# Kernel optimization log

Hardware: AMD Instinct MI355X
Metric: run time of the kernel (lower is better)

Reference implementation:

```python
import jax, jax.numpy as jnp
import numpy as np

B, L, D = 1, 4096, 1024
H = 16
HD = D // H
SCALE = HD ** -0.5


def setup_inputs() -> dict:
    key = jax.random.key(0)
    k1, k2, k3 = jax.random.split(key, 3)
    X = jax.random.normal(k1, (B, L, D), dtype=jnp.float32)
    # torch Linear default init ~ U(-1/sqrt(fan_in), 1/sqrt(fan_in)); scaled normals are fine for a reference
    Wqkv = jax.random.normal(k2, (D, 3 * D), dtype=jnp.float32) * (D ** -0.5)
    bqkv = jnp.zeros((3 * D,), dtype=jnp.float32)
    Wproj = jax.random.normal(k3, (D, D), dtype=jnp.float32) * (D ** -0.5)
    bproj = jnp.zeros((D,), dtype=jnp.float32)
    return {"X": X, "Wqkv": Wqkv, "bqkv": bqkv, "Wproj": Wproj, "bproj": bproj}


def reference(X, Wqkv, bqkv, Wproj, bproj):
    Bn, Ln, Dn = X.shape
    qkv = X @ Wqkv + bqkv                       # [B, L, 3D]
    qkv = qkv.reshape(Bn, Ln, 3, H, HD)
    q, k, v = qkv[:, :, 0], qkv[:, :, 1], qkv[:, :, 2]   # [B, L, H, HD]
    # attention scores [B, H, L, L] (naive, matches original)
    attn = jnp.einsum('bqhd,bkhd->bhqk', q, k) * SCALE
    causal = jnp.tril(jnp.ones((Ln, Ln), dtype=bool))     # True = keep
    attn = jnp.where(causal, attn, -jnp.inf)
    score = jax.nn.softmax(attn, axis=-1)
    out = jnp.einsum('bhqk,bkhd->bqhd', score, v)         # [B, L, H, HD]
    out = out.reshape(Bn, Ln, Dn)
    return out @ Wproj + bproj
```

## Files before the change

### kernel.cpp

```cpp
#include <hip/hip_runtime.h>
#include <hip/hip_bf16.h>
#include <string.h>


typedef unsigned short ushort_t;
typedef __attribute__((ext_vector_type(8))) short short8;
typedef __attribute__((ext_vector_type(4))) short short4_t;
typedef __attribute__((ext_vector_type(4))) float f32x4;

#define MFMA16(a, b, c) __builtin_amdgcn_mfma_f32_16x16x32_bf16(a, b, c, 0, 0, 0)

#if __has_builtin(__builtin_amdgcn_mfma_f32_16x16x16bf16_1k)
#define HAVE_MFMA16K 1
__device__ __forceinline__ f32x4 mfma16x16(short4_t a, short4_t b, f32x4 c) {
    return __builtin_amdgcn_mfma_f32_16x16x16bf16_1k(a, b, c, 0, 0, 0);
}
#else
#define HAVE_MFMA16K 0
__device__ __forceinline__ f32x4 mfma16x16(short4_t a, short4_t b, f32x4 c) {
    asm("s_nop 1\n\tv_mfma_f32_16x16x16_bf16 %0, %1, %2, %0"
        : "+v"(c) : "v"(a), "v"(b));
    return c;
}
#endif

static constexpr int Lq = 4096;
static constexpr int Dm = 1024;
static constexpr int NH = 16;
static constexpr int HD = 64;
static constexpr int D3 = 3072;
static constexpr float SCALE_LOG2E = 0.125f * 1.44269504088896340736f;

__device__ __forceinline__ ushort_t f2bf(float f) {
    union { float f; unsigned int u; } x{f};
    unsigned int u = x.u;
    u += 0x7fffu + ((u >> 16) & 1u);
    return (ushort_t)(u >> 16);
}

__device__ __forceinline__ unsigned int cvtpk(float a, float b) {
    __hip_bfloat162 h = __float22bfloat162_rn(make_float2(a, b));
    unsigned int u;
    memcpy(&u, &h, 4);
    return u;
}

__device__ __forceinline__ void gl2lds16(const ushort_t* g, ushort_t* l) {
    __builtin_amdgcn_global_load_lds(
        (const __attribute__((address_space(1))) unsigned int*)g,
        (__attribute__((address_space(3))) unsigned int*)l, 16, 0, 0);
}

__global__ void __launch_bounds__(256)
prep(const float* __restrict__ X, const float* __restrict__ Wqkv,
     const float* __restrict__ Wproj, ushort_t* __restrict__ Xb,
     ushort_t* __restrict__ WqkvT, ushort_t* __restrict__ WprojT) {
    __shared__ float tile[32][33];
    const int bid = blockIdx.x, tid = threadIdx.x;
    if (bid < 4096) {
        int i = (bid * 256 + tid) * 4;
        float4 v = *(const float4*)&X[i];
        ushort_t r[4] = { f2bf(v.x), f2bf(v.y), f2bf(v.z), f2bf(v.w) };
        *(uint2*)&Xb[i] = *(uint2*)r;
        return;
    }
    const float* W; ushort_t* Wt; int Nd, nb, kb;
    if (bid < 7168) {
        int b = bid - 4096; W = Wqkv;  Wt = WqkvT;  Nd = 3072;
        nb = (b % 96) * 32; kb = (b / 96) * 32;
    } else {
        int b = bid - 7168; W = Wproj; Wt = WprojT; Nd = 1024;
        nb = (b % 32) * 32; kb = (b / 32) * 32;
    }
    const int tx = tid & 31, ty = tid >> 5;
    for (int j = 0; j < 32; j += 8)
        tile[ty + j][tx] = W[(size_t)(kb + ty + j) * Nd + nb + tx];
    __syncthreads();
    for (int j = 0; j < 32; j += 8)
        Wt[(size_t)(nb + ty + j) * Dm + kb + tx] = f2bf(tile[tx][ty + j]);
}

__global__ void __launch_bounds__(256)
gemm_qkv(const ushort_t* __restrict__ A, const ushort_t* __restrict__ Bt,
         const float* __restrict__ bias, ushort_t* __restrict__ Cq,
         ushort_t* __restrict__ Vt) {
    __shared__ alignas(16) ushort_t Alds[128 * 32];
    __shared__ alignas(16) ushort_t Blds[128 * 32];
    const int tid  = threadIdx.x;
    const int lane = tid & 63;
    const int w    = tid >> 6;
    const int quad = lane >> 4;
    const int l16  = lane & 15;
    const int mbase = blockIdx.x * 128;
    const int nbase = blockIdx.y * 128;
    const int moff  = (w >> 1) * 64;
    const int noff  = (w & 1) * 64;
    const int K = Dm;

    f32x4 acc[4][4] = {};

    for (int kb = 0; kb < K; kb += 32) {
        __syncthreads();
        #pragma unroll
        for (int c = 0; c < 2; c++) {
            int id  = w * 128 + c * 64 + lane;
            int row = id >> 2, col = (id & 3) * 8;
            gl2lds16(&A[(size_t)(mbase + row) * K + kb + col], &Alds[(size_t)(w * 128 + c * 64) * 8]);
            gl2lds16(&Bt[(size_t)(nbase + row) * K + kb + col], &Blds[(size_t)(w * 128 + c * 64) * 8]);
        }
        __syncthreads();
        short8 a[4], b[4];
        #pragma unroll
        for (int m = 0; m < 4; m++)
            a[m] = *(const short8*)&Alds[(moff + m * 16 + l16) * 32 + quad * 8];
        #pragma unroll
        for (int n = 0; n < 4; n++)
            b[n] = *(const short8*)&Blds[(noff + n * 16 + l16) * 32 + quad * 8];
        #pragma unroll
        for (int m = 0; m < 4; m++)
            #pragma unroll
            for (int n = 0; n < 4; n++)
                acc[m][n] = MFMA16(a[m], b[n], acc[m][n]);
    }

    if (nbase < 2048) {
        const bool qscale = (nbase < 1024);
        #pragma unroll
        for (int m = 0; m < 4; m++)
            #pragma unroll
            for (int n = 0; n < 4; n++)
                #pragma unroll
                for (int r = 0; r < 4; r++) {
                    int row = mbase + moff + m * 16 + quad * 4 + r;
                    int col = nbase + noff + n * 16 + l16;
                    float v = acc[m][n][r] + bias[col];
                    if (qscale) v *= SCALE_LOG2E;
                    Cq[(size_t)row * D3 + col] = f2bf(v);
                }
    } else {
        const int dbase = nbase - 2048 + noff;
        const size_t kb0 = (size_t)mbase + moff;
        #pragma unroll
        for (int n = 0; n < 4; n++) {
            const float bv = bias[nbase + noff + n * 16 + l16];
            ushort_t* vrow = Vt + (size_t)(dbase + n * 16 + l16) * Lq + kb0 + quad * 16;
            #pragma unroll
            for (int rp = 0; rp < 2; rp++) {
                ushort_t pk[8];
                #pragma unroll
                for (int dr = 0; dr < 2; dr++)
                    #pragma unroll
                    for (int m = 0; m < 4; m++)
                        pk[dr * 4 + m] = f2bf(acc[m][n][2 * rp + dr] + bv);
                *(short8*)(vrow + rp * 8) = *(const short8*)pk;
            }
        }
    }
}

__global__ void __launch_bounds__(1024)
attn_fwd(const ushort_t* __restrict__ qkv, const ushort_t* __restrict__ Vt,
         ushort_t* __restrict__ O) {
    union SMem {
        struct { ushort_t K[2][2][64 * 64]; ushort_t V[2][2][64 * 64]; } kv;
        float Ml[3 * 256 * 35];
    };
    __shared__ SMem sm;

    const int tid  = threadIdx.x;
    const int lane = tid & 63;
    const int w    = tid >> 6;
    const int qtr  = w >> 2;
    const int sub  = w & 3;
    const int quad = lane >> 4;
    const int l16  = lane & 15;
    const int bid  = blockIdx.x;
    const int h    = bid & 15;
    const int p    = bid >> 4;
    const float NEG_INF = -__builtin_inff();

    const ushort_t* kbase = qkv + Dm + h * HD;
    const ushort_t* vbase = Vt + (size_t)h * HD * Lq;

    int koff[2][2];
    #pragma unroll
    for (int s = 0; s < 2; s++) {
        const int tok = (l16 & 3) * 16 + (qtr & 1) * 8 + s * 4 + (l16 >> 2);
        const int fk  = ((l16 & 3) << 1) | ((l16 >> 2) & 1);
        #pragma unroll
        for (int kh = 0; kh < 2; kh++)
            koff[s][kh] = tok * 64 + (((kh * 4 + quad) ^ fk) * 8);
    }
    int voff[4][2];
    #pragma unroll
    for (int t4 = 0; t4 < 4; t4++)
        #pragma unroll
        for (int s = 0; s < 2; s++) {
            const int row = t4 * 16 + l16;
            const int g = (qtr & 1) * 4 + s * 2 + (quad >> 1);
            voff[t4][s] = row * 64 + ((g ^ (l16 & 7)) * 8) + (quad & 1) * 4;
        }
    const int kmc = (qtr >> 1) * 64 + (qtr & 1) * 8 + quad;

    const int  tv  = tid & 511;
    const int  rr  = tv >> 3;
    const int  ccK = (tv & 7) ^ ((((rr >> 4) & 3) << 1) | (rr & 1));
    const int  ccV = (tv & 7) ^ (rr & 7);
    const bool isK = (tid < 512);
    const int  dsto = (w & 7) * 512;
    const ushort_t* kse = kbase + (size_t)rr * D3 + ccK * 8;
    const ushort_t* vse = vbase + (size_t)rr * Lq + ccV * 8;

    for (int sel = 0; sel < 2; sel++) {
        const int c      = sel ? (31 - p) : p;
        const int qc     = c * 128;
        const int rounds = c + 1;
        const int qrow0  = qc + sub * 32;

        short8 qf[2][2];
        #pragma unroll
        for (int m = 0; m < 2; m++) {
            const ushort_t* qr = qkv + (size_t)(qrow0 + m * 16 + l16) * D3 + h * HD;
            qf[m][0] = *(const short8*)(qr + quad * 8);
            qf[m][1] = *(const short8*)(qr + 32 + quad * 8);
        }

        f32x4 o[2][4] = {};
        float sacc[2] = { 0.f, 0.f };

        const ushort_t* kp = kse;
        const ushort_t* vp = vse;

        auto stage = [&](int b) {
            if (isK) {
                gl2lds16(kp,           &sm.kv.K[0][b][dsto]);
                gl2lds16(kp + 64 * D3, &sm.kv.K[1][b][dsto]);
            } else {
                gl2lds16(vp,           &sm.kv.V[0][b][dsto]);
                gl2lds16(vp + 64,      &sm.kv.V[1][b][dsto]);
            }
            kp += (size_t)128 * D3;
            vp += 128;
        };

        stage(0);

        for (int r = 0; r < rounds; r++) {
            const int buf = r & 1;
            __syncthreads();
            if (r + 1 < rounds) stage(buf ^ 1);

            const ushort_t* Kb = &sm.kv.K[qtr >> 1][buf][0];
            const ushort_t* Vb = &sm.kv.V[qtr >> 1][buf][0];
            const bool domask = (r == rounds - 1);

            short8 kf[2][2];
            #pragma unroll
            for (int s = 0; s < 2; s++)
                #pragma unroll
                for (int kh = 0; kh < 2; kh++)
                    kf[s][kh] = *(const short8*)&Kb[koff[s][kh]];

            short4_t pT[2][2];
            #pragma unroll
            for (int m = 0; m < 2; m++) {
                const int qg = qrow0 + m * 16 + l16;
                #pragma unroll
                for (int s = 0; s < 2; s++) {
                    f32x4 t = {};
                    t = MFMA16(kf[s][0], qf[m][0], t);
                    t = MFMA16(kf[s][1], qf[m][1], t);
                    float e[4];
                    #pragma unroll
                    for (int r4 = 0; r4 < 4; r4++) {
                        float v = t[r4];
                        if (domask && (r * 128 + kmc + s * 4 + r4 * 16 > qg))
                            v = NEG_INF;
                        e[r4] = __builtin_amdgcn_exp2f(v);
                    }
                    sacc[m] += (e[0] + e[1]) + (e[2] + e[3]);
                    union { unsigned int u[2]; short4_t s4; } pb;
                    pb.u[0] = cvtpk(e[0], e[1]);
                    pb.u[1] = cvtpk(e[2], e[3]);
                    pT[m][s] = pb.s4;
                }
            }

            #pragma unroll
            for (int t4 = 0; t4 < 4; t4++)
                #pragma unroll
                for (int s = 0; s < 2; s++) {
                    short4_t vf = *(const short4_t*)&Vb[voff[t4][s]];
                    o[0][t4] = mfma16x16(vf, pT[0][s], o[0][t4]);
                    o[1][t4] = mfma16x16(vf, pT[1][s], o[1][t4]);
                }
        }

#if !HAVE_MFMA16K
        asm volatile("s_nop 7\n\ts_nop 7" ::: "memory");
#endif
        #pragma unroll
        for (int m = 0; m < 2; m++) {
            sacc[m] += __shfl_xor(sacc[m], 16);
            sacc[m] += __shfl_xor(sacc[m], 32);
        }

        __syncthreads();
        if (qtr != 0) {
            float* dst = sm.Ml + (size_t)((qtr - 1) * 256 + sub * 64 + lane) * 35;
            #pragma unroll
            for (int m = 0; m < 2; m++)
                #pragma unroll
                for (int t4 = 0; t4 < 4; t4++)
                    *(f32x4*)(dst + (m * 4 + t4) * 4) = o[m][t4];
            dst[32] = sacc[0];
            dst[33] = sacc[1];
        }
        __syncthreads();
        if (qtr == 0) {
            #pragma unroll
            for (int j = 0; j < 3; j++) {
                const float* src = sm.Ml + (size_t)(j * 256 + sub * 64 + lane) * 35;
                #pragma unroll
                for (int m = 0; m < 2; m++)
                    #pragma unroll
                    for (int t4 = 0; t4 < 4; t4++)
                        o[m][t4] += *(const f32x4*)(src + (m * 4 + t4) * 4);
                sacc[0] += src[32];
                sacc[1] += src[33];
            }
            #pragma unroll
            for (int m = 0; m < 2; m++) {
                const float inv = 1.0f / sacc[m];
                ushort_t* orow = O + (size_t)(qrow0 + m * 16 + l16) * Dm + h * HD;
                #pragma unroll
                for (int t4 = 0; t4 < 4; t4++) {
                    ushort_t pk[4];
                    #pragma unroll
                    for (int r4 = 0; r4 < 4; r4++)
                        pk[r4] = f2bf(o[m][t4][r4] * inv);
                    *(uint2*)(orow + t4 * 16 + quad * 4) = *(const uint2*)pk;
                }
            }
        }
        __syncthreads();
    }
}

__global__ void __launch_bounds__(256)
gemm_proj(const ushort_t* __restrict__ A, const ushort_t* __restrict__ Bt,
          const float* __restrict__ bias, float* __restrict__ C) {
    __shared__ alignas(16) ushort_t Alds[128 * 32];
    __shared__ alignas(16) ushort_t Blds[64 * 32];
    const int tid  = threadIdx.x;
    const int lane = tid & 63;
    const int w    = tid >> 6;
    const int quad = lane >> 4;
    const int l16  = lane & 15;
    const int mbase = blockIdx.x * 128;
    const int nbase = blockIdx.y * 64;
    const int moff  = (w >> 1) * 64;
    const int noff  = (w & 1) * 32;
    const int K = Dm, N = Dm;

    f32x4 acc[4][2] = {};

    for (int kb = 0; kb < K; kb += 32) {
        __syncthreads();
        #pragma unroll
        for (int c = 0; c < 2; c++) {
            int id  = w * 128 + c * 64 + lane;
            int row = id >> 2, col = (id & 3) * 8;
            gl2lds16(&A[(size_t)(mbase + row) * K + kb + col], &Alds[(size_t)(w * 128 + c * 64) * 8]);
        }
        {
            int id  = w * 64 + lane;
            int row = id >> 2, col = (id & 3) * 8;
            gl2lds16(&Bt[(size_t)(nbase + row) * K + kb + col], &Blds[(size_t)(w * 64) * 8]);
        }
        __syncthreads();
        short8 a[4], b[2];
        #pragma unroll
        for (int m = 0; m < 4; m++)
            a[m] = *(const short8*)&Alds[(moff + m * 16 + l16) * 32 + quad * 8];
        #pragma unroll
        for (int n = 0; n < 2; n++)
            b[n] = *(const short8*)&Blds[(noff + n * 16 + l16) * 32 + quad * 8];
        #pragma unroll
        for (int m = 0; m < 4; m++)
            #pragma unroll
            for (int n = 0; n < 2; n++)
                acc[m][n] = MFMA16(a[m], b[n], acc[m][n]);
    }

    #pragma unroll
    for (int m = 0; m < 4; m++)
        #pragma unroll
        for (int n = 0; n < 2; n++)
            #pragma unroll
            for (int r = 0; r < 4; r++) {
                int row = mbase + moff + m * 16 + quad * 4 + r;
                int col = nbase + noff + n * 16 + l16;
                C[(size_t)row * N + col] = acc[m][n][r] + bias[col];
            }
}

extern "C" void kernel_launch(void* const* d_in, const int* in_sizes, int n_in,
                              void* d_out, int out_size, void* d_ws, size_t ws_size,
                              hipStream_t stream) {
    const float* X     = (const float*)d_in[0];
    const float* Wqkv  = (const float*)d_in[1];
    const float* bqkv  = (const float*)d_in[2];
    const float* Wproj = (const float*)d_in[3];
    const float* bproj = (const float*)d_in[4];
    float* out = (float*)d_out;

    ushort_t* ws     = (ushort_t*)d_ws;
    ushort_t* Xb     = ws;
    ushort_t* WqkvT  = Xb + (size_t)Lq * Dm;
    ushort_t* WprojT = WqkvT + (size_t)D3 * Dm;
    ushort_t* qkvB   = WprojT + (size_t)Dm * Dm;
    ushort_t* VtB    = qkvB + (size_t)Lq * D3;
    ushort_t* Ob     = VtB + (size_t)NH * HD * Lq;

    prep<<<dim3(8192), 256, 0, stream>>>(X, Wqkv, Wproj, Xb, WqkvT, WprojT);

    gemm_qkv<<<dim3(Lq / 128, D3 / 128), 256, 0, stream>>>(
        Xb, WqkvT, bqkv, qkvB, VtB);

    attn_fwd<<<dim3(256), 1024, 0, stream>>>(qkvB, VtB, Ob);

    gemm_proj<<<dim3(Lq / 128, Dm / 64), 256, 0, stream>>>(
        Ob, WprojT, bproj, out);
}
```

Measured before the change: 211.7 us.

## Hoist V LDS loads, batch QK MFMAs with setprio, change V swizzle, use pk cvt

Within the attention inner loop, all V fragment reads from LDS are now issued early, alongside the K reads, so their latency overlaps the QK^T MFMAs and the softmax exp work. The QK MFMAs are grouped into one block ahead of the exp step, and both MFMA phases are wrapped in s_setprio to favour matrix issue across waves. The V LDS swizzle gains an extra XOR term on row bit 3 to reduce bank conflicts, and bf16 packing now uses the v_cvt_pk_bf16_f32 instruction directly. Holding the preloaded V fragments and the score tiles raises register pressure.

```diff
diff --git a/kernel.cpp b/kernel.cpp
--- a/kernel.cpp
+++ b/kernel.cpp
@@ -39,10 +39,9 @@
 }
 
 __device__ __forceinline__ unsigned int cvtpk(float a, float b) {
-    __hip_bfloat162 h = __float22bfloat162_rn(make_float2(a, b));
-    unsigned int u;
-    memcpy(&u, &h, 4);
-    return u;
+    unsigned int r;
+    asm("v_cvt_pk_bf16_f32 %0, %1, %2" : "=v"(r) : "v"(a), "v"(b));
+    return r;
 }
 
 __device__ __forceinline__ void gl2lds16(const ushort_t* g, ushort_t* l) {
@@ -198,14 +197,15 @@
         for (int s = 0; s < 2; s++) {
             const int row = t4 * 16 + l16;
             const int g = (qtr & 1) * 4 + s * 2 + (quad >> 1);
-            voff[t4][s] = row * 64 + ((g ^ (l16 & 7)) * 8) + (quad & 1) * 4;
+            const int sx = (row & 7) ^ (((row >> 3) & 1) << 2);
+            voff[t4][s] = row * 64 + ((g ^ sx) * 8) + (quad & 1) * 4;
         }
     const int kmc = (qtr >> 1) * 64 + (qtr & 1) * 8 + quad;
 
     const int  tv  = tid & 511;
     const int  rr  = tv >> 3;
     const int  ccK = (tv & 7) ^ ((((rr >> 4) & 3) << 1) | (rr & 1));
-    const int  ccV = (tv & 7) ^ (rr & 7);
+    const int  ccV = (tv & 7) ^ ((rr & 7) ^ (((rr >> 3) & 1) << 2));
     const bool isK = (tid < 512);
     const int  dsto = (w & 7) * 512;
     const ushort_t* kse = kbase + (size_t)rr * D3 + ccK * 8;
@@ -260,20 +260,36 @@
                 #pragma unroll
                 for (int kh = 0; kh < 2; kh++)
                     kf[s][kh] = *(const short8*)&Kb[koff[s][kh]];
-
-            short4_t pT[2][2];
-            #pragma unroll
-            for (int m = 0; m < 2; m++) {
-                const int qg = qrow0 + m * 16 + l16;
+            short4_t vf[4][2];
+            #pragma unroll
+            for (int t4 = 0; t4 < 4; t4++)
+                #pragma unroll
+                for (int s = 0; s < 2; s++)
+                    vf[t4][s] = *(const short4_t*)&Vb[voff[t4][s]];
+
+            f32x4 st[2][2];
+            __builtin_amdgcn_s_setprio(1);
+            #pragma unroll
+            for (int m = 0; m < 2; m++)
                 #pragma unroll
                 for (int s = 0; s < 2; s++) {
                     f32x4 t = {};
                     t = MFMA16(kf[s][0], qf[m][0], t);
                     t = MFMA16(kf[s][1], qf[m][1], t);
+                    st[m][s] = t;
+                }
+            __builtin_amdgcn_s_setprio(0);
+
+            short4_t pT[2][2];
+            #pragma unroll
+            for (int m = 0; m < 2; m++) {
+                const int qg = qrow0 + m * 16 + l16;
+                #pragma unroll
+                for (int s = 0; s < 2; s++) {
                     float e[4];
                     #pragma unroll
                     for (int r4 = 0; r4 < 4; r4++) {
-                        float v = t[r4];
+                        float v = st[m][s][r4];
                         if (domask && (r * 128 + kmc + s * 4 + r4 * 16 > qg))
                             v = NEG_INF;
                         e[r4] = __builtin_amdgcn_exp2f(v);
@@ -286,14 +302,15 @@
                 }
             }
 
+            __builtin_amdgcn_s_setprio(1);
             #pragma unroll
             for (int t4 = 0; t4 < 4; t4++)
                 #pragma unroll
                 for (int s = 0; s < 2; s++) {
-                    short4_t vf = *(const short4_t*)&Vb[voff[t4][s]];
-                    o[0][t4] = mfma16x16(vf, pT[0][s], o[0][t4]);
-                    o[1][t4] = mfma16x16(vf, pT[1][s], o[1][t4]);
+                    o[0][t4] = mfma16x16(vf[t4][s], pT[0][s], o[0][t4]);
+                    o[1][t4] = mfma16x16(vf[t4][s], pT[1][s], o[1][t4]);
                 }
+            __builtin_amdgcn_s_setprio(0);
         }
 
 #if !HAVE_MFMA16K
```

Result: faster. 205.6 us (-2.9%).
